# Kernel optimization log

Measured on AMD Instinct MI355X. Metric: run time of the kernel, lower is better.

Reference implementation:

```python
import jax, jax.numpy as jnp
import numpy as np

D = 1024      # embed_size
H = 16        # num_heads
NEXP = 8      # num_experts
TOPK = 3
THRESH = 0.05
COEF = 0.01
B, SQ, SKV = 4, 1024, 1024


def _ln(x, g, b, eps=1e-5):
    m = jnp.mean(x, axis=-1, keepdims=True)
    v = jnp.mean(jnp.square(x - m), axis=-1, keepdims=True)
    return (x - m) * jax.lax.rsqrt(v + eps) * g + b


def setup_inputs() -> dict:
    key = jax.random.key(0)
    ks = jax.random.split(key, 20)
    s = 0.02
    w = lambda k, shape: (jax.random.normal(k, shape, jnp.float32) * s)
    return {
        'query': jax.random.normal(ks[0], (B, SQ, D), jnp.float32),
        'key_value': jax.random.normal(ks[1], (B, SKV, D), jnp.float32),
        'Wq': w(ks[2], (D, D)), 'bq': jnp.zeros((D,), jnp.float32),
        'Wk': w(ks[3], (D, D)), 'bk': jnp.zeros((D,), jnp.float32),
        'Wv': w(ks[4], (D, D)), 'bv': jnp.zeros((D,), jnp.float32),
        'W_in': w(ks[5], (3 * D, D)), 'b_in': jnp.zeros((3 * D,), jnp.float32),
        'W_out': w(ks[6], (D, D)), 'b_out': jnp.zeros((D,), jnp.float32),
        'Wa': w(ks[7], (D, D)), 'ba': jnp.zeros((D,), jnp.float32),
        'ln1_g': jnp.ones((D,), jnp.float32), 'ln1_b': jnp.zeros((D,), jnp.float32),
        'Wg': w(ks[8], (D, NEXP)),
        'ew1': w(ks[9], (NEXP, D, 4 * D)), 'eb1': jnp.zeros((NEXP, 4 * D), jnp.float32),
        'ew2': w(ks[10], (NEXP, 4 * D, D)), 'eb2': jnp.zeros((NEXP, D), jnp.float32),
        'ln2_g': jnp.ones((D,), jnp.float32), 'ln2_b': jnp.zeros((D,), jnp.float32),
    }


def reference(query, key_value, Wq, bq, Wk, bk, Wv, bv, W_in, b_in, W_out, b_out,
              Wa, ba, ln1_g, ln1_b, Wg, ew1, eb1, ew2, eb2, ln2_g, ln2_b):
    Bq, Sq, _ = query.shape
    Skv = key_value.shape[1]
    Dh = D // H
    # outer Q/K/V linears (torch Linear: x @ W.T + b)
    q = query @ Wq.T + bq
    k = key_value @ Wk.T + bk
    v = key_value @ Wv.T + bv
    # nn.MultiheadAttention in-projection
    Wiq, Wik, Wiv = jnp.split(W_in, 3, axis=0)
    biq, bik, biv = jnp.split(b_in, 3)
    qh = (q @ Wiq.T + biq).reshape(Bq, Sq, H, Dh).transpose(0, 2, 1, 3)
    kh = (k @ Wik.T + bik).reshape(Bq, Skv, H, Dh).transpose(0, 2, 1, 3)
    vh = (v @ Wiv.T + biv).reshape(Bq, Skv, H, Dh).transpose(0, 2, 1, 3)
    scores = jnp.einsum('bhqd,bhkd->bhqk', qh, kh) / jnp.sqrt(jnp.float32(Dh))
    attn = jax.nn.softmax(scores, axis=-1)
    o = jnp.einsum('bhqk,bhkd->bhqd', attn, vh).transpose(0, 2, 1, 3).reshape(Bq, Sq, D)
    o = o @ W_out.T + b_out
    # adapt + residual + first_norm
    x = _ln(o @ Wa.T + ba + query, ln1_g, ln1_b)
    # ---- MoE: top-3 softmax gating, threshold on non-top-1 gates ----
    probs = jax.nn.softmax(x @ Wg, axis=-1)                 # [B,S,E]
    topv, topi = jax.lax.top_k(probs, TOPK)                  # [B,S,3]
    keep = jnp.concatenate([jnp.ones_like(topv[..., :1], bool),
                            topv[..., 1:] >= THRESH], axis=-1)
    topv = jnp.where(keep, topv, 0.0)
    combine = jnp.sum(jax.nn.one_hot(topi, NEXP, dtype=x.dtype) * topv[..., None], axis=-2)  # [B,S,E]
    moe_out = jnp.zeros_like(x)
    for e in range(NEXP):  # small fixed expert count
        h = jax.nn.gelu(x @ ew1[e] + eb1[e], approximate=False)
        moe_out = moe_out + combine[..., e:e + 1] * (h @ ew2[e] + eb2[e])
    # load-balance aux loss: E * sum(frac_routed * mean_prob) * coef
    fe = jnp.mean((combine > 0).astype(x.dtype), axis=(0, 1))
    me = jnp.mean(probs, axis=(0, 1))
    aux = COEF * NEXP * jnp.sum(fe * me)
    out = _ln(moe_out + x, ln2_g, ln2_b)
    return out, aux
```

## Files before the change

### kernel.cpp

```cpp
#include <hip/hip_runtime.h>
#include <math.h>

#define THRESH_C 0.05f
#define COEF_C   0.01f

typedef __bf16 bf16;
typedef __bf16 bf16x8 __attribute__((ext_vector_type(8)));
typedef __bf16 bf16x4 __attribute__((ext_vector_type(4)));
typedef float  f32x4  __attribute__((ext_vector_type(4)));

__device__ __forceinline__ void ld16(void* lds_base, const void* g) {
    __builtin_amdgcn_global_load_lds(
        (const __attribute__((address_space(1))) void*)g,
        (__attribute__((address_space(3))) void*)lds_base,
        16, 0, 0);
}

__global__ __launch_bounds__(256) void k_f32_to_split(const float* __restrict__ in,
                                                      bf16* __restrict__ hi,
                                                      bf16* __restrict__ lo, long n) {
    long i = ((long)blockIdx.x * 256 + threadIdx.x) * 4;
    if (i >= n) return;
    float4 v = *(const float4*)(in + i);
    bf16x4 h, l;
    h[0] = (bf16)v.x; l[0] = (bf16)(v.x - (float)h[0]);
    h[1] = (bf16)v.y; l[1] = (bf16)(v.y - (float)h[1]);
    h[2] = (bf16)v.z; l[2] = (bf16)(v.z - (float)h[2]);
    h[3] = (bf16)v.w; l[3] = (bf16)(v.w - (float)h[3]);
    *(bf16x4*)(hi + i) = h;
    *(bf16x4*)(lo + i) = l;
}

__global__ __launch_bounds__(256) void k_transpose4_split(const float* __restrict__ w0,
                                                          const float* __restrict__ w1,
                                                          const float* __restrict__ w2,
                                                          const float* __restrict__ w3,
                                                          bf16* __restrict__ oh,
                                                          bf16* __restrict__ ol) {
    __shared__ float t[64][65];
    int z = blockIdx.z;
    const float* in = (z == 0) ? w0 : (z == 1) ? w1 : (z == 2) ? w2 : w3;
    bf16* ohz = oh + (long)z * 1048576;
    bf16* olz = ol + (long)z * 1048576;
    int r0 = blockIdx.y * 64, c0 = blockIdx.x * 64;
    for (int i = threadIdx.x; i < 4096; i += 256) {
        int r = i >> 6, c = i & 63;
        t[r][c] = in[(long)(r0 + r) * 1024 + (c0 + c)];
    }
    __syncthreads();
    for (int i = threadIdx.x; i < 4096; i += 256) {
        int c = i >> 6, r = i & 63;
        float v = t[r][c];
        bf16 h = (bf16)v;
        long o = (long)(c0 + c) * 1024 + (r0 + r);
        ohz[o] = h;
        olz[o] = (bf16)(v - (float)h);
    }
}

__global__ __launch_bounds__(256) void k_transpose_ew(const float* __restrict__ in,
                                                      bf16* __restrict__ out,
                                                      int R, int C) {
    __shared__ bf16 t[64][65];
    const float* ib = in + (long)blockIdx.z * R * C;
    bf16* ob = out + (long)blockIdx.z * R * C;
    int r0 = blockIdx.y * 64, c0 = blockIdx.x * 64;
    for (int i = threadIdx.x; i < 4096; i += 256) {
        int r = i >> 6, c = i & 63;
        t[r][c] = (bf16)ib[(long)(r0 + r) * C + (c0 + c)];
    }
    __syncthreads();
    for (int i = threadIdx.x; i < 4096; i += 256) {
        int c = i >> 6, r = i & 63;
        ob[(long)(c0 + c) * R + (r0 + r)] = t[r][c];
    }
}

__global__ __launch_bounds__(256) void k_bias_fold4(const float* __restrict__ W_in,
                                                    const float* __restrict__ Wa,
                                                    const float* __restrict__ bq,
                                                    const float* __restrict__ bk,
                                                    const float* __restrict__ bv,
                                                    const float* __restrict__ b_out,
                                                    const float* __restrict__ b_in,
                                                    const float* __restrict__ ba,
                                                    float* __restrict__ y) {
    int z = blockIdx.y;
    const float* W  = (z < 3) ? (W_in + (long)z * 1048576) : Wa;
    const float* b1 = (z == 0) ? bq : (z == 1) ? bk : (z == 2) ? bv : b_out;
    const float* b2 = (z < 3) ? (b_in + z * 1024) : ba;
    int row = blockIdx.x * 4 + (threadIdx.x >> 6);
    int lane = threadIdx.x & 63;
    const float* wr = W + (long)row * 1024;
    float s = 0.f;
    for (int k = lane; k < 1024; k += 64) s += wr[k] * b1[k];
#pragma unroll
    for (int o = 32; o >= 1; o >>= 1) s += __shfl_xor(s, o);
    if (lane == 0) y[z * 1024 + row] = b2[row] + s;
}

enum { HP_SPLIT = 0, HP_F32 = 1, HP_SPLIT_HEADS = 2 };

template<int MODE>
__global__ __launch_bounds__(256)
void gemm_hp(const bf16* __restrict__ Ah, const bf16* __restrict__ Al, int lda, long sAz,
             const bf16* __restrict__ Bh, const bf16* __restrict__ Bl, int ldb, long sBz,
             void* __restrict__ Chv, bf16* __restrict__ Cl, int ldc, long sCz,
             const float* __restrict__ bias, float alpha, int M, int N, int K) {
    __shared__ alignas(16) bf16 sAh[128 * 32];
    __shared__ alignas(16) bf16 sAl[128 * 32];
    __shared__ alignas(16) bf16 sBh[128 * 32];
    __shared__ alignas(16) bf16 sBl[128 * 32];
    const int bm = blockIdx.y, bn = blockIdx.x, z = blockIdx.z;
    const int tid  = threadIdx.x;
    const int lane = tid & 63, wave = tid >> 6;
    const int quad = lane >> 4, l16 = lane & 15;
    const int wr = wave >> 1, wc = wave & 1;
    const int sr = tid >> 2;
    const int sc = (tid & 3) * 8;

    int arow0 = min(bm * 128 + sr, M - 1);
    int arow1 = min(bm * 128 + sr + 64, M - 1);
    int brow0 = min(bn * 128 + sr, N - 1);
    int brow1 = min(bn * 128 + sr + 64, N - 1);

    const bf16* pAh0 = Ah + (long)z * sAz + (long)arow0 * lda + sc;
    const bf16* pAh1 = Ah + (long)z * sAz + (long)arow1 * lda + sc;
    const bf16* pAl0 = Al + (long)z * sAz + (long)arow0 * lda + sc;
    const bf16* pAl1 = Al + (long)z * sAz + (long)arow1 * lda + sc;
    const bf16* pBh0 = Bh + (long)z * sBz + (long)brow0 * ldb + sc;
    const bf16* pBh1 = Bh + (long)z * sBz + (long)brow1 * ldb + sc;
    const bf16* pBl0 = Bl + (long)z * sBz + (long)brow0 * ldb + sc;
    const bf16* pBl1 = Bl + (long)z * sBz + (long)brow1 * ldb + sc;
    const int wo = wave << 9;

    f32x4 acc[4][4];
#pragma unroll
    for (int i = 0; i < 4; i++)
#pragma unroll
        for (int j = 0; j < 4; j++) acc[i][j] = (f32x4){0.f, 0.f, 0.f, 0.f};

    for (int k0 = 0; k0 < K; k0 += 32) {
        __syncthreads();
        ld16(sAh + wo,        pAh0 + k0);
        ld16(sAh + 2048 + wo, pAh1 + k0);
        ld16(sAl + wo,        pAl0 + k0);
        ld16(sAl + 2048 + wo, pAl1 + k0);
        ld16(sBh + wo,        pBh0 + k0);
        ld16(sBh + 2048 + wo, pBh1 + k0);
        ld16(sBl + wo,        pBl0 + k0);
        ld16(sBl + 2048 + wo, pBl1 + k0);
        __syncthreads();
        bf16x8 ah[4], al[4], bh[4], bl[4];
#pragma unroll
        for (int i = 0; i < 4; i++) {
            int ro = (wr * 64 + i * 16 + l16) * 32 + quad * 8;
            ah[i] = *(const bf16x8*)&sAh[ro];
            al[i] = *(const bf16x8*)&sAl[ro];
        }
#pragma unroll
        for (int j = 0; j < 4; j++) {
            int ro = (wc * 64 + j * 16 + l16) * 32 + quad * 8;
            bh[j] = *(const bf16x8*)&sBh[ro];
            bl[j] = *(const bf16x8*)&sBl[ro];
        }
#pragma unroll
        for (int i = 0; i < 4; i++)
#pragma unroll
            for (int j = 0; j < 4; j++) {
                acc[i][j] = __builtin_amdgcn_mfma_f32_16x16x32_bf16(al[i], bh[j], acc[i][j], 0, 0, 0);
                acc[i][j] = __builtin_amdgcn_mfma_f32_16x16x32_bf16(ah[i], bl[j], acc[i][j], 0, 0, 0);
                acc[i][j] = __builtin_amdgcn_mfma_f32_16x16x32_bf16(ah[i], bh[j], acc[i][j], 0, 0, 0);
            }
    }

#pragma unroll
    for (int i = 0; i < 4; i++) {
        int mbase = bm * 128 + wr * 64 + i * 16 + quad * 4;
#pragma unroll
        for (int j = 0; j < 4; j++) {
            int n = bn * 128 + wc * 64 + j * 16 + l16;
            if (n < N) {
                float bv = bias ? bias[n] : 0.f;
#pragma unroll
                for (int r = 0; r < 4; r++) {
                    int m = mbase + r;
                    if (m < M) {
                        float v = alpha * acc[i][j][r] + bv;
                        if (MODE == HP_SPLIT) {
                            long cidx = (long)z * sCz + (long)m * ldc + n;
                            bf16 h = (bf16)v;
                            ((bf16*)Chv)[cidx] = h;
                            Cl[cidx] = (bf16)(v - (float)h);
                        } else if (MODE == HP_F32) {
                            long cidx = (long)z * sCz + (long)m * ldc + n;
                            ((float*)Chv)[cidx] = v;
                        } else {
                            int slice = ((m >> 10) << 4) + (n >> 6);
                            long idx = (long)slice * 65536 + (long)(m & 1023) * 64 + (n & 63);
                            bf16 h = (bf16)v;
                            ((bf16*)Chv)[idx] = h;
                            Cl[idx] = (bf16)(v - (float)h);
                        }
                    }
                }
            }
        }
    }
}

__global__ __launch_bounds__(256)
void gemm_pv(const bf16* __restrict__ Ph, const bf16* __restrict__ Pl,
             const bf16* __restrict__ Vh, const bf16* __restrict__ Vl,
             bf16* __restrict__ Oh, bf16* __restrict__ Ol) {
    __shared__ alignas(16) bf16 sAh[128 * 32];
    __shared__ alignas(16) bf16 sAl[128 * 32];
    __shared__ alignas(16) bf16 sBh[64 * 32];
    __shared__ alignas(16) bf16 sBl[64 * 32];
    const int bm = blockIdx.x, z = blockIdx.y;
    const int tid = threadIdx.x, lane = tid & 63, wave = tid >> 6;
    const int quad = lane >> 4, l16 = lane & 15;
    const int wr = wave & 1, wc = wave >> 1;
    const int sr = tid >> 2, sc = (tid & 3) * 8;

    const bf16* pA0h = Ph + (long)z * 1048576 + (long)(bm * 128 + sr) * 1024 + sc;
    const bf16* pA1h = pA0h + 64 * 1024;
    const bf16* pA0l = Pl + (long)z * 1048576 + (long)(bm * 128 + sr) * 1024 + sc;
    const bf16* pA1l = pA0l + 64 * 1024;
    const bf16* pB0h = Vh + (long)z * 65536 + (long)sr * 1024 + sc;
    const bf16* pB0l = Vl + (long)z * 65536 + (long)sr * 1024 + sc;
    const int wo = wave << 9;
    const int wob = wave << 7;

    f32x4 acc[4][2];
#pragma unroll
    for (int i = 0; i < 4; i++)
#pragma unroll
        for (int j = 0; j < 2; j++) acc[i][j] = (f32x4){0.f, 0.f, 0.f, 0.f};

    for (int k0 = 0; k0 < 1024; k0 += 32) {
        __syncthreads();
        ld16(sAh + wo,        pA0h + k0);
        ld16(sAh + 2048 + wo, pA1h + k0);
        ld16(sAl + wo,        pA0l + k0);
        ld16(sAl + 2048 + wo, pA1l + k0);
        ld16(sBh + wo, pB0h + k0);
        ld16(sBl + wo, pB0l + k0);
        __syncthreads();
        bf16x8 ah[4], al[4], bh[2], bl[2];
#pragma unroll
        for (int i = 0; i < 4; i++) {
            int ro = (wr * 64 + i * 16 + l16) * 32 + quad * 8;
            ah[i] = *(const bf16x8*)&sAh[ro];
            al[i] = *(const bf16x8*)&sAl[ro];
        }
#pragma unroll
        for (int j = 0; j < 2; j++) {
            int ro = (wc * 32 + j * 16 + l16) * 32 + quad * 8;
            bh[j] = *(const bf16x8*)&sBh[ro];
            bl[j] = *(const bf16x8*)&sBl[ro];
        }
#pragma unroll
        for (int i = 0; i < 4; i++)
#pragma unroll
            for (int j = 0; j < 2; j++) {
                acc[i][j] = __builtin_amdgcn_mfma_f32_16x16x32_bf16(al[i], bh[j], acc[i][j], 0, 0, 0);
                acc[i][j] = __builtin_amdgcn_mfma_f32_16x16x32_bf16(ah[i], bl[j], acc[i][j], 0, 0, 0);
                acc[i][j] = __builtin_amdgcn_mfma_f32_16x16x32_bf16(ah[i], bh[j], acc[i][j], 0, 0, 0);
            }
    }

#pragma unroll
    for (int i = 0; i < 4; i++) {
        int mbase = bm * 128 + wr * 64 + i * 16 + quad * 4;
#pragma unroll
        for (int j = 0; j < 2; j++) {
            int n = wc * 32 + j * 16 + l16;
#pragma unroll
            for (int r = 0; r < 4; r++) {
                int m = mbase + r;
                long idx = (long)z * 65536 + (long)m * 64 + n;
                float v = acc[i][j][r];
                bf16 h = (bf16)v;
                Oh[idx] = h;
                Ol[idx] = (bf16)(v - (float)h);
            }
        }
    }
}

__global__ __launch_bounds__(256)
void gemm_moe1(const bf16* __restrict__ Ae, const bf16* __restrict__ ew1t,
               const float* __restrict__ eb1, bf16* __restrict__ Hp,
               const int* __restrict__ counts, const int* __restrict__ bases) {
    const int e = blockIdx.z;
    const int M = counts[e];
    const int bm = blockIdx.y, bn = blockIdx.x;
    if (bm * 128 >= M) return;
    const bf16* A = Ae + (long)bases[e] * 1024;
    const bf16* B = ew1t + (long)e * 4194304;
    bf16* C = Hp + (long)bases[e] * 4096;
    const float* bias = eb1 + e * 4096;

    __shared__ alignas(16) bf16 sA[128 * 32];
    __shared__ alignas(16) bf16 sB[128 * 32];
    const int tid  = threadIdx.x;
    const int lane = tid & 63, wave = tid >> 6;
    const int quad = lane >> 4, l16 = lane & 15;
    const int wr = wave >> 1, wc = wave & 1;
    const int sr = tid >> 2;
    const int sc = (tid & 3) * 8;

    int arow0 = min(bm * 128 + sr, M - 1);
    int arow1 = min(bm * 128 + sr + 64, M - 1);
    int brow0 = bn * 128 + sr;
    const bf16* pA0 = A + (long)arow0 * 1024 + sc;
    const bf16* pA1 = A + (long)arow1 * 1024 + sc;
    const bf16* pB0 = B + (long)brow0 * 1024 + sc;
    const bf16* pB1 = B + (long)(brow0 + 64) * 1024 + sc;
    const int wo = wave << 9;

    f32x4 acc[4][4];
#pragma unroll
    for (int i = 0; i < 4; i++)
#pragma unroll
        for (int j = 0; j < 4; j++) acc[i][j] = (f32x4){0.f, 0.f, 0.f, 0.f};

    for (int k0 = 0; k0 < 1024; k0 += 32) {
        __syncthreads();
        ld16(sA + wo,        pA0 + k0);
        ld16(sA + 2048 + wo, pA1 + k0);
        ld16(sB + wo,        pB0 + k0);
        ld16(sB + 2048 + wo, pB1 + k0);
        __syncthreads();
        bf16x8 af[4], bfr[4];
#pragma unroll
        for (int i = 0; i < 4; i++)
            af[i] = *(const bf16x8*)&sA[(wr * 64 + i * 16 + l16) * 32 + quad * 8];
#pragma unroll
        for (int j = 0; j < 4; j++)
            bfr[j] = *(const bf16x8*)&sB[(wc * 64 + j * 16 + l16) * 32 + quad * 8];
#pragma unroll
        for (int i = 0; i < 4; i++)
#pragma unroll
            for (int j = 0; j < 4; j++)
                acc[i][j] = __builtin_amdgcn_mfma_f32_16x16x32_bf16(af[i], bfr[j], acc[i][j], 0, 0, 0);
    }

#pragma unroll
    for (int i = 0; i < 4; i++) {
        int mbase = bm * 128 + wr * 64 + i * 16 + quad * 4;
#pragma unroll
        for (int j = 0; j < 4; j++) {
            int n = bn * 128 + wc * 64 + j * 16 + l16;
            float bv = bias[n];
#pragma unroll
            for (int r = 0; r < 4; r++) {
                int m = mbase + r;
                if (m < M) {
                    float v = acc[i][j][r] + bv;
                    float g = 0.5f * v * (1.f + erff(v * 0.70710678118654752f));
                    C[(long)m * 4096 + n] = (bf16)g;
                }
            }
        }
    }
}

__global__ __launch_bounds__(256)
void gemm_moe2(const bf16* __restrict__ Hp, const bf16* __restrict__ ew2t,
               const float* __restrict__ eb2, float* __restrict__ moe_out,
               const int* __restrict__ counts, const int* __restrict__ bases,
               const int* __restrict__ tok, const float* __restrict__ combine) {
    const int e = blockIdx.z;
    const int M = counts[e];
    const int ks = blockIdx.y & 3;
    const int bm = blockIdx.y >> 2;
    const int bn = blockIdx.x;
    if (bm * 128 >= M) return;
    const bf16* A = Hp + (long)bases[e] * 4096 + ks * 1024;
    const bf16* B = ew2t + (long)e * 4194304 + ks * 1024;
    const float* bias = eb2 + e * 1024;
    const int* etok = tok + e * 4096;

    __shared__ alignas(16) bf16 sA[128 * 32];
    __shared__ alignas(16) bf16 sB[128 * 32];
    const int tid  = threadIdx.x;
    const int lane = tid & 63, wave = tid >> 6;
    const int quad = lane >> 4, l16 = lane & 15;
    const int wr = wave >> 1, wc = wave & 1;
    const int sr = tid >> 2;
    const int sc = (tid & 3) * 8;

    int arow0 = min(bm * 128 + sr, M - 1);
    int arow1 = min(bm * 128 + sr + 64, M - 1);
    int brow0 = bn * 128 + sr;
    const bf16* pA0 = A + (long)arow0 * 4096 + sc;
    const bf16* pA1 = A + (long)arow1 * 4096 + sc;
    const bf16* pB0 = B + (long)brow0 * 4096 + sc;
    const bf16* pB1 = B + (long)(brow0 + 64) * 4096 + sc;
    const int wo = wave << 9;

    f32x4 acc[4][4];
#pragma unroll
    for (int i = 0; i < 4; i++)
#pragma unroll
        for (int j = 0; j < 4; j++) acc[i][j] = (f32x4){0.f, 0.f, 0.f, 0.f};

    for (int k0 = 0; k0 < 1024; k0 += 32) {
        __syncthreads();
        ld16(sA + wo,        pA0 + k0);
        ld16(sA + 2048 + wo, pA1 + k0);
        ld16(sB + wo,        pB0 + k0);
        ld16(sB + 2048 + wo, pB1 + k0);
        __syncthreads();
        bf16x8 af[4], bfr[4];
#pragma unroll
        for (int i = 0; i < 4; i++)
            af[i] = *(const bf16x8*)&sA[(wr * 64 + i * 16 + l16) * 32 + quad * 8];
#pragma unroll
        for (int j = 0; j < 4; j++)
            bfr[j] = *(const bf16x8*)&sB[(wc * 64 + j * 16 + l16) * 32 + quad * 8];
#pragma unroll
        for (int i = 0; i < 4; i++)
#pragma unroll
            for (int j = 0; j < 4; j++)
                acc[i][j] = __builtin_amdgcn_mfma_f32_16x16x32_bf16(af[i], bfr[j], acc[i][j], 0, 0, 0);
    }

#pragma unroll
    for (int i = 0; i < 4; i++) {
        int mbase = bm * 128 + wr * 64 + i * 16 + quad * 4;
#pragma unroll
        for (int j = 0; j < 4; j++) {
            int n = bn * 128 + wc * 64 + j * 16 + l16;
            float bv = (ks == 0) ? bias[n] : 0.f;
#pragma unroll
            for (int r = 0; r < 4; r++) {
                int m = mbase + r;
                if (m < M) {
                    int t = etok[m];
                    float s = combine[t * 8 + e];
                    atomicAdd(&moe_out[(long)t * 1024 + n], s * (acc[i][j][r] + bv));
                }
            }
        }
    }
}

__global__ __launch_bounds__(256) void k_vsplit(const bf16* __restrict__ VH_h,
                                                const bf16* __restrict__ VH_l,
                                                bf16* __restrict__ VT_h,
                                                bf16* __restrict__ VT_l) {
    __shared__ bf16 th[64][65];
    __shared__ bf16 tl[64][65];
    int s = blockIdx.y, q0 = blockIdx.x * 64;
    int b = s >> 4, h = s & 15;
    long ibase = ((long)(b * 1024 + q0)) * 1024 + h * 64;
    for (int i = threadIdx.x; i < 4096; i += 256) {
        int q = i >> 6, d = i & 63;
        th[q][d] = VH_h[ibase + (long)q * 1024 + d];
        tl[q][d] = VH_l[ibase + (long)q * 1024 + d];
    }
    __syncthreads();
    long obase = (long)s * 65536 + q0;
    for (int i = threadIdx.x; i < 4096; i += 256) {
        int d = i >> 6, q = i & 63;
        VT_h[obase + (long)d * 1024 + q] = th[q][d];
        VT_l[obase + (long)d * 1024 + q] = tl[q][d];
    }
}

__global__ __launch_bounds__(256) void k_ocopy(const bf16* __restrict__ Op_h,
                                               const bf16* __restrict__ Op_l,
                                               bf16* __restrict__ O_h,
                                               bf16* __restrict__ O_l) {
    int t = blockIdx.x * 4 + (threadIdx.x >> 6);
    int lane = threadIdx.x & 63;
    int b = t >> 10, q = t & 1023;
    int h = lane >> 2, dd = (lane & 3) * 16;
    long src = ((long)(b * 16 + h)) * 65536 + (long)q * 64 + dd;
    long dst = (long)t * 1024 + h * 64 + dd;
    *(bf16x8*)(O_h + dst)     = *(const bf16x8*)(Op_h + src);
    *(bf16x8*)(O_h + dst + 8) = *(const bf16x8*)(Op_h + src + 8);
    *(bf16x8*)(O_l + dst)     = *(const bf16x8*)(Op_l + src);
    *(bf16x8*)(O_l + dst + 8) = *(const bf16x8*)(Op_l + src + 8);
}

__global__ __launch_bounds__(256) void k_gather(const bf16* __restrict__ Xb,
                                                const int* __restrict__ tok,
                                                const int* __restrict__ counts,
                                                const int* __restrict__ bases,
                                                bf16* __restrict__ Ae) {
    int e = blockIdx.y;
    int cnt = counts[e];
    long base = bases[e];
    for (int i = blockIdx.x; i < cnt; i += gridDim.x) {
        int t = tok[e * 4096 + i];
        const bf16x4* src = (const bf16x4*)(Xb + (long)t * 1024);
        bf16x4* dst = (bf16x4*)(Ae + (base + i) * 1024);
        dst[threadIdx.x] = src[threadIdx.x];
    }
}

__global__ __launch_bounds__(256) void k_softmax_ip(bf16* __restrict__ Sh,
                                                    bf16* __restrict__ Sl) {
    int row = blockIdx.x * 4 + (threadIdx.x >> 6);
    int lane = threadIdx.x & 63;
    long o = (long)row * 1024 + lane * 16;
    bf16x8 h0 = *(const bf16x8*)(Sh + o), h1 = *(const bf16x8*)(Sh + o + 8);
    bf16x8 l0 = *(const bf16x8*)(Sl + o), l1 = *(const bf16x8*)(Sl + o + 8);
    float v[16];
#pragma unroll
    for (int i = 0; i < 8; i++) {
        v[i] = (float)h0[i] + (float)l0[i];
        v[8 + i] = (float)h1[i] + (float)l1[i];
    }
    float mx = v[0];
#pragma unroll
    for (int i = 1; i < 16; i++) mx = fmaxf(mx, v[i]);
#pragma unroll
    for (int of = 32; of >= 1; of >>= 1) mx = fmaxf(mx, __shfl_xor(mx, of));
    float s = 0.f;
#pragma unroll
    for (int i = 0; i < 16; i++) { v[i] = expf(v[i] - mx); s += v[i]; }
#pragma unroll
    for (int of = 32; of >= 1; of >>= 1) s += __shfl_xor(s, of);
    float inv = 1.f / s;
#pragma unroll
    for (int i = 0; i < 8; i++) {
        float a = v[i] * inv;
        h0[i] = (bf16)a; l0[i] = (bf16)(a - (float)h0[i]);
        float b = v[8 + i] * inv;
        h1[i] = (bf16)b; l1[i] = (bf16)(b - (float)h1[i]);
    }
    *(bf16x8*)(Sh + o) = h0;  *(bf16x8*)(Sh + o + 8) = h1;
    *(bf16x8*)(Sl + o) = l0;  *(bf16x8*)(Sl + o + 8) = l1;
}

__global__ __launch_bounds__(256) void k_ln(const float* __restrict__ xin,
                                            const float* __restrict__ resid,
                                            const float* __restrict__ g,
                                            const float* __restrict__ bb,
                                            float* __restrict__ outf,
                                            bf16* __restrict__ outb) {
    int row = blockIdx.x * 4 + (threadIdx.x >> 6);
    int lane = threadIdx.x & 63;
    long base = (long)row * 1024 + lane * 16;
    float v[16];
#pragma unroll
    for (int i = 0; i < 16; i += 4) {
        f32x4 a = *(const f32x4*)(xin + base + i);
        if (resid) { f32x4 r4 = *(const f32x4*)(resid + base + i); a += r4; }
        v[i] = a[0]; v[i + 1] = a[1]; v[i + 2] = a[2]; v[i + 3] = a[3];
    }
    float s = 0.f;
#pragma unroll
    for (int i = 0; i < 16; i++) s += v[i];
#pragma unroll
    for (int o = 32; o >= 1; o >>= 1) s += __shfl_xor(s, o);
    float mean = s * (1.f / 1024.f);
    float vs = 0.f;
#pragma unroll
    for (int i = 0; i < 16; i++) { float d = v[i] - mean; vs += d * d; }
#pragma unroll
    for (int o = 32; o >= 1; o >>= 1) vs += __shfl_xor(vs, o);
    float inv = 1.f / sqrtf(vs * (1.f / 1024.f) + 1e-5f);
    const float* gp = g + lane * 16;
    const float* bp = bb + lane * 16;
#pragma unroll
    for (int i = 0; i < 16; i++) {
        float o = (v[i] - mean) * inv * gp[i] + bp[i];
        if (outf) outf[base + i] = o;
        if (outb) outb[base + i] = (bf16)o;
    }
}

__global__ __launch_bounds__(256) void k_gate(const float* __restrict__ X,
                                              const float* __restrict__ Wg,
                                              float* __restrict__ combine,
                                              float* __restrict__ partials) {
    __shared__ float sm[16];
    if (threadIdx.x < 16) sm[threadIdx.x] = 0.f;
    __syncthreads();
    int t = blockIdx.x * 4 + (threadIdx.x >> 6);
    int lane = threadIdx.x & 63;
    const float* x = X + (long)t * 1024;
    float acc[8] = {0.f, 0.f, 0.f, 0.f, 0.f, 0.f, 0.f, 0.f};
    for (int i = lane; i < 1024; i += 64) {
        float xv = x[i];
        const float* w = Wg + i * 8;
#pragma unroll
        for (int e = 0; e < 8; e++) acc[e] += xv * w[e];
    }
#pragma unroll
    for (int e = 0; e < 8; e++)
#pragma unroll
        for (int o = 32; o >= 1; o >>= 1) acc[e] += __shfl_xor(acc[e], o);
    if (lane == 0) {
        float mx = acc[0];
#pragma unroll
        for (int e = 1; e < 8; e++) mx = fmaxf(mx, acc[e]);
        float p[8], s = 0.f;
#pragma unroll
        for (int e = 0; e < 8; e++) { p[e] = expf(acc[e] - mx); s += p[e]; }
        float invs = 1.f / s;
#pragma unroll
        for (int e = 0; e < 8; e++) p[e] *= invs;
        float b1 = -1.f, b2 = -1.f, b3 = -1.f; int i1 = 0, i2 = 0, i3 = 0;
#pragma unroll
        for (int e = 0; e < 8; e++) {
            float pe = p[e];
            if (pe > b1)      { b3 = b2; i3 = i2; b2 = b1; i2 = i1; b1 = pe; i1 = e; }
            else if (pe > b2) { b3 = b2; i3 = i2; b2 = pe; i2 = e; }
            else if (pe > b3) { b3 = pe; i3 = e; }
        }
        float c[8] = {0.f, 0.f, 0.f, 0.f, 0.f, 0.f, 0.f, 0.f};
        c[i1] = b1;
        if (b2 >= THRESH_C) c[i2] = b2;
        if (b3 >= THRESH_C) c[i3] = b3;
        float* co = combine + (long)t * 8;
#pragma unroll
        for (int e = 0; e < 8; e++) co[e] = c[e];
#pragma unroll
        for (int e = 0; e < 8; e++) {
            atomicAdd(&sm[e], p[e]);
            if (c[e] > 0.f) atomicAdd(&sm[8 + e], 1.f);
        }
    }
    __syncthreads();
    if (threadIdx.x < 16) partials[(long)blockIdx.x * 16 + threadIdx.x] = sm[threadIdx.x];
}

__global__ __launch_bounds__(256) void k_route(const float* __restrict__ combine,
                                               int* __restrict__ counts,
                                               int* __restrict__ bases,
                                               int* __restrict__ tok) {
    __shared__ int scan[256];
    __shared__ int ebase;
    int tid = threadIdx.x;
    if (tid == 0) ebase = 0;
    __syncthreads();
    for (int e = 0; e < 8; e++) {
        int pred[16]; int cnt = 0;
#pragma unroll
        for (int j = 0; j < 16; j++) {
            int t = tid * 16 + j;
            pred[j] = combine[t * 8 + e] > 0.f ? 1 : 0;
            cnt += pred[j];
        }
        scan[tid] = cnt;
        __syncthreads();
        for (int off = 1; off < 256; off <<= 1) {
            int v = (tid >= off) ? scan[tid - off] : 0;
            __syncthreads();
            scan[tid] += v;
            __syncthreads();
        }
        int o = e * 4096 + scan[tid] - cnt;
        int total = scan[255];
#pragma unroll
        for (int j = 0; j < 16; j++) {
            if (pred[j]) tok[o++] = tid * 16 + j;
        }
        if (tid == 0) { counts[e] = total; bases[e] = ebase; ebase += total; }
        __syncthreads();
    }
}

__global__ __launch_bounds__(256) void k_aux(const float* __restrict__ partials, int nblocks,
                                             float* __restrict__ auxout) {
    __shared__ float red[256];
    int tid = threadIdx.x;
    int e = tid & 15, grp = tid >> 4;
    float s = 0.f;
    for (int b = grp; b < nblocks; b += 16) s += partials[(long)b * 16 + e];
    red[tid] = s;
    __syncthreads();
    if (grp == 0) {
        float tot = 0.f;
        for (int g2 = 0; g2 < 16; g2++) tot += red[g2 * 16 + e];
        red[tid] = tot;
    }
    __syncthreads();
    if (tid == 0) {
        float s2 = 0.f;
        for (int e2 = 0; e2 < 8; e2++)
            s2 += (red[8 + e2] * (1.f / 4096.f)) * (red[e2] * (1.f / 4096.f));
        auxout[0] = COEF_C * 8.f * s2;
    }
}

extern "C" void kernel_launch(void* const* d_in, const int* in_sizes, int n_in,
                              void* d_out, int out_size, void* d_ws, size_t ws_size,
                              hipStream_t stream) {
    const float* query     = (const float*)d_in[0];
    const float* key_value = (const float*)d_in[1];
    const float* Wq   = (const float*)d_in[2];
    const float* bq   = (const float*)d_in[3];
    const float* Wk   = (const float*)d_in[4];
    const float* bk   = (const float*)d_in[5];
    const float* Wv   = (const float*)d_in[6];
    const float* bv   = (const float*)d_in[7];
    const float* W_in = (const float*)d_in[8];
    const float* b_in = (const float*)d_in[9];
    const float* W_out = (const float*)d_in[10];
    const float* b_out = (const float*)d_in[11];
    const float* Wa   = (const float*)d_in[12];
    const float* ba   = (const float*)d_in[13];
    const float* ln1_g = (const float*)d_in[14];
    const float* ln1_b = (const float*)d_in[15];
    const float* Wg   = (const float*)d_in[16];
    const float* ew1  = (const float*)d_in[17];
    const float* eb1  = (const float*)d_in[18];
    const float* ew2  = (const float*)d_in[19];
    const float* eb2  = (const float*)d_in[20];
    const float* ln2_g = (const float*)d_in[21];
    const float* ln2_b = (const float*)d_in[22];

    const size_t MBY = 1ull << 20;
    const long MB1 = 1024L * 1024L;
    char* ws = (char*)d_ws;

    bf16* Sh   = (bf16*)(ws + 0 * MBY);
    bf16* Sl   = (bf16*)(ws + 64 * MBY);
    bf16* ew1t = (bf16*)(ws + 0 * MBY);
    bf16* ew2t = (bf16*)(ws + 64 * MBY);
    bf16* WAll_h = (bf16*)(ws + 128 * MBY);
    bf16* WAll_l = (bf16*)(ws + 136 * MBY);
    bf16* WT_h   = (bf16*)(ws + 144 * MBY);
    bf16* WT_l   = (bf16*)(ws + 152 * MBY);
    bf16* Xq_h  = (bf16*)(ws + 160 * MBY), *Xq_l  = (bf16*)(ws + 168 * MBY);
    bf16* Xkv_h = (bf16*)(ws + 176 * MBY), *Xkv_l = (bf16*)(ws + 184 * MBY);
    bf16* O_h  = (bf16*)(ws + 160 * MBY), *O_l  = (bf16*)(ws + 168 * MBY);
    bf16* QHp_h = (bf16*)(ws + 192 * MBY), *QHp_l = (bf16*)(ws + 200 * MBY);
    bf16* KHp_h = (bf16*)(ws + 208 * MBY), *KHp_l = (bf16*)(ws + 216 * MBY);
    bf16* VH_h  = (bf16*)(ws + 224 * MBY), *VH_l  = (bf16*)(ws + 232 * MBY);
    bf16* VTp_h = (bf16*)(ws + 240 * MBY), *VTp_l = (bf16*)(ws + 248 * MBY);
    bf16* Op_h  = (bf16*)(ws + 256 * MBY), *Op_l  = (bf16*)(ws + 264 * MBY);
    float* Xf   = (float*)(ws + 256 * MBY);
    float* Af   = (float*)(ws + 272 * MBY);
    bf16* Ae      = (bf16*)(ws + 128 * MBY);
    bf16* Hp      = (bf16*)(ws + 152 * MBY);
    float* moe_out = (float*)(ws + 272 * MBY);
    bf16* Xb   = (bf16*)(ws + 320 * MBY);
    bf16* Weff_h = (bf16*)(ws + 328 * MBY);
    bf16* Weff_l = (bf16*)(ws + 336 * MBY);
    float* combine  = (float*)(ws + 344 * MBY);
    float* partials = (float*)(ws + 344 * MBY + 128 * 1024);
    float* beff     = (float*)(ws + 344 * MBY + 192 * 1024);
    int*   counts   = (int*)  (ws + 344 * MBY + 212 * 1024);
    int*   bases    = (int*)  (ws + 344 * MBY + 213 * 1024);
    int*   tok      = (int*)  (ws + 344 * MBY + 214 * 1024);

    dim3 blk(256);

    k_f32_to_split<<<4096, blk, 0, stream>>>(query, Xq_h, Xq_l, 4L * MB1);
    k_f32_to_split<<<4096, blk, 0, stream>>>(key_value, Xkv_h, Xkv_l, 4L * MB1);
    k_f32_to_split<<<3072, blk, 0, stream>>>(W_in, WAll_h, WAll_l, 3L * MB1);
    k_f32_to_split<<<1024, blk, 0, stream>>>(Wa, WAll_h + 3 * MB1, WAll_l + 3 * MB1, MB1);
    k_transpose4_split<<<dim3(16, 16, 4), blk, 0, stream>>>(Wq, Wk, Wv, W_out, WT_h, WT_l);
    k_bias_fold4<<<dim3(256, 4), blk, 0, stream>>>(W_in, Wa, bq, bk, bv, b_out, b_in, ba, beff);

    gemm_hp<HP_SPLIT><<<dim3(8, 8, 4), blk, 0, stream>>>(
        WAll_h, WAll_l, 1024, MB1, WT_h, WT_l, 1024, MB1,
        Weff_h, Weff_l, 1024, MB1, nullptr, 1.f, 1024, 1024, 1024);

    dim3 gP(8, 32, 1);
    gemm_hp<HP_SPLIT_HEADS><<<gP, blk, 0, stream>>>(Xq_h, Xq_l, 1024, 0, Weff_h, Weff_l, 1024, 0,
                                                    QHp_h, QHp_l, 0, 0, beff, 1.f, 4096, 1024, 1024);
    gemm_hp<HP_SPLIT_HEADS><<<gP, blk, 0, stream>>>(Xkv_h, Xkv_l, 1024, 0, Weff_h + MB1, Weff_l + MB1, 1024, 0,
                                                    KHp_h, KHp_l, 0, 0, beff + 1024, 1.f, 4096, 1024, 1024);
    gemm_hp<HP_SPLIT><<<gP, blk, 0, stream>>>(Xkv_h, Xkv_l, 1024, 0, Weff_h + 2 * MB1, Weff_l + 2 * MB1, 1024, 0,
                                              VH_h, VH_l, 1024, 0, beff + 2048, 1.f, 4096, 1024, 1024);
    k_vsplit<<<dim3(16, 64), blk, 0, stream>>>(VH_h, VH_l, VTp_h, VTp_l);

    for (int half = 0; half < 2; half++) {
        long so = (long)half * 32 * 65536;
        gemm_hp<HP_SPLIT><<<dim3(8, 8, 32), blk, 0, stream>>>(
            QHp_h + so, QHp_l + so, 64, 65536,
            KHp_h + so, KHp_l + so, 64, 65536,
            Sh, Sl, 1024, MB1, nullptr, 0.125f, 1024, 1024, 64);
        k_softmax_ip<<<8192, blk, 0, stream>>>(Sh, Sl);
        gemm_pv<<<dim3(8, 32), blk, 0, stream>>>(Sh, Sl, VTp_h + so, VTp_l + so,
                                                 Op_h + so, Op_l + so);
    }
    k_ocopy<<<1024, blk, 0, stream>>>(Op_h, Op_l, O_h, O_l);

    gemm_hp<HP_F32><<<gP, blk, 0, stream>>>(O_h, O_l, 1024, 0, Weff_h + 3 * MB1, Weff_l + 3 * MB1, 1024, 0,
                                            Af, nullptr, 1024, 0, beff + 3072, 1.f, 4096, 1024, 1024);
    k_ln<<<1024, blk, 0, stream>>>(Af, query, ln1_g, ln1_b, Xf, Xb);
    k_gate<<<1024, blk, 0, stream>>>(Xf, Wg, combine, partials);
    k_route<<<1, blk, 0, stream>>>(combine, counts, bases, tok);
    k_gather<<<dim3(512, 8), blk, 0, stream>>>(Xb, tok, counts, bases, Ae);

    k_transpose_ew<<<dim3(64, 16, 8), blk, 0, stream>>>(ew1, ew1t, 1024, 4096);
    k_transpose_ew<<<dim3(16, 64, 8), blk, 0, stream>>>(ew2, ew2t, 4096, 1024);

    hipMemsetAsync(moe_out, 0, (long)4096 * 1024 * 4, stream);
    gemm_moe1<<<dim3(32, 32, 8), blk, 0, stream>>>(Ae, ew1t, eb1, Hp, counts, bases);
    gemm_moe2<<<dim3(8, 128, 8), blk, 0, stream>>>(Hp, ew2t, eb2, moe_out, counts, bases, tok, combine);

    k_ln<<<1024, blk, 0, stream>>>(moe_out, Xf, ln2_g, ln2_b, (float*)d_out, nullptr);
    k_aux<<<1, blk, 0, stream>>>(partials, 1024, (float*)d_out + (out_size - 1));
}
```

Before: 1.751 ms.

## Replace atomic scatter in MoE down-projection with dense store and fused combine+LayerNorm

The second expert GEMM no longer splits K four ways and scatters weighted results into moe_out with float atomics. It now runs the full K=4096 reduction per tile and writes plain per-expert rows into a compacted buffer. The router also emits a token-to-slot map, which a new kernel uses to gather each token's expert outputs, add bias, apply the gate weights and the residual, and run LayerNorm. This removes the memset and the atomic traffic, but the GEMM grid is four times smaller and each block runs a longer K loop, so there is less parallelism.

```diff
diff --git a/kernel.cpp b/kernel.cpp
--- a/kernel.cpp
+++ b/kernel.cpp
@@ -230,7 +230,6 @@
     const bf16* pB0h = Vh + (long)z * 65536 + (long)sr * 1024 + sc;
     const bf16* pB0l = Vl + (long)z * 65536 + (long)sr * 1024 + sc;
     const int wo = wave << 9;
-    const int wob = wave << 7;
 
     f32x4 acc[4][2];
 #pragma unroll
@@ -369,19 +368,16 @@
 
 __global__ __launch_bounds__(256)
 void gemm_moe2(const bf16* __restrict__ Hp, const bf16* __restrict__ ew2t,
-               const float* __restrict__ eb2, float* __restrict__ moe_out,
-               const int* __restrict__ counts, const int* __restrict__ bases,
-               const int* __restrict__ tok, const float* __restrict__ combine) {
+               float* __restrict__ Y,
+               const int* __restrict__ counts, const int* __restrict__ bases) {
     const int e = blockIdx.z;
     const int M = counts[e];
-    const int ks = blockIdx.y & 3;
-    const int bm = blockIdx.y >> 2;
+    const int bm = blockIdx.y;
     const int bn = blockIdx.x;
     if (bm * 128 >= M) return;
-    const bf16* A = Hp + (long)bases[e] * 4096 + ks * 1024;
-    const bf16* B = ew2t + (long)e * 4194304 + ks * 1024;
-    const float* bias = eb2 + e * 1024;
-    const int* etok = tok + e * 4096;
+    const bf16* A = Hp + (long)bases[e] * 4096;
+    const bf16* B = ew2t + (long)e * 4194304;
+    float* C = Y + (long)bases[e] * 1024;
 
     __shared__ alignas(16) bf16 sA[128 * 32];
     __shared__ alignas(16) bf16 sB[128 * 32];
@@ -407,7 +403,7 @@
 #pragma unroll
         for (int j = 0; j < 4; j++) acc[i][j] = (f32x4){0.f, 0.f, 0.f, 0.f};
 
-    for (int k0 = 0; k0 < 1024; k0 += 32) {
+    for (int k0 = 0; k0 < 4096; k0 += 32) {
         __syncthreads();
         ld16(sA + wo,        pA0 + k0);
         ld16(sA + 2048 + wo, pA1 + k0);
@@ -434,15 +430,10 @@
 #pragma unroll
         for (int j = 0; j < 4; j++) {
             int n = bn * 128 + wc * 64 + j * 16 + l16;
-            float bv = (ks == 0) ? bias[n] : 0.f;
 #pragma unroll
             for (int r = 0; r < 4; r++) {
                 int m = mbase + r;
-                if (m < M) {
-                    int t = etok[m];
-                    float s = combine[t * 8 + e];
-                    atomicAdd(&moe_out[(long)t * 1024 + n], s * (acc[i][j][r] + bv));
-                }
+                if (m < M) C[(long)m * 1024 + n] = acc[i][j][r];
             }
         }
     }
@@ -576,6 +567,59 @@
     }
 }
 
+__global__ __launch_bounds__(256) void k_moe_ln(const float* __restrict__ Y,
+                                                const int* __restrict__ pos,
+                                                const float* __restrict__ combine,
+                                                const float* __restrict__ eb2,
+                                                const float* __restrict__ resid,
+                                                const float* __restrict__ g,
+                                                const float* __restrict__ bb,
+                                                float* __restrict__ outf) {
+    int row = blockIdx.x * 4 + (threadIdx.x >> 6);
+    int lane = threadIdx.x & 63;
+    long base = (long)row * 1024 + lane * 16;
+    float v[16];
+#pragma unroll
+    for (int i = 0; i < 16; i += 4) {
+        f32x4 a = *(const f32x4*)(resid + base + i);
+        v[i] = a[0]; v[i + 1] = a[1]; v[i + 2] = a[2]; v[i + 3] = a[3];
+    }
+    for (int e = 0; e < 8; e++) {
+        int p = pos[row * 8 + e];
+        if (p >= 0) {
+            float c = combine[row * 8 + e];
+            const float* yr = Y + (long)p * 1024 + lane * 16;
+            const float* br = eb2 + e * 1024 + lane * 16;
+#pragma unroll
+            for (int i = 0; i < 16; i += 4) {
+                f32x4 y4 = *(const f32x4*)(yr + i);
+                f32x4 b4 = *(const f32x4*)(br + i);
+                v[i]     += c * (y4[0] + b4[0]);
+                v[i + 1] += c * (y4[1] + b4[1]);
+                v[i + 2] += c * (y4[2] + b4[2]);
+                v[i + 3] += c * (y4[3] + b4[3]);
+            }
+        }
+    }
+    float s = 0.f;
+#pragma unroll
+    for (int i = 0; i < 16; i++) s += v[i];
+#pragma unroll
+    for (int o = 32; o >= 1; o >>= 1) s += __shfl_xor(s, o);
+    float mean = s * (1.f / 1024.f);
+    float vs = 0.f;
+#pragma unroll
+    for (int i = 0; i < 16; i++) { float d = v[i] - mean; vs += d * d; }
+#pragma unroll
+    for (int o = 32; o >= 1; o >>= 1) vs += __shfl_xor(vs, o);
+    float inv = 1.f / sqrtf(vs * (1.f / 1024.f) + 1e-5f);
+    const float* gp = g + lane * 16;
+    const float* bp = bb + lane * 16;
+#pragma unroll
+    for (int i = 0; i < 16; i++)
+        outf[base + i] = (v[i] - mean) * inv * gp[i] + bp[i];
+}
+
 __global__ __launch_bounds__(256) void k_gate(const float* __restrict__ X,
                                               const float* __restrict__ Wg,
                                               float* __restrict__ combine,
@@ -635,12 +679,11 @@
 __global__ __launch_bounds__(256) void k_route(const float* __restrict__ combine,
                                                int* __restrict__ counts,
                                                int* __restrict__ bases,
-                                               int* __restrict__ tok) {
+                                               int* __restrict__ tok,
+                                               int* __restrict__ pos) {
     __shared__ int scan[256];
-    __shared__ int ebase;
     int tid = threadIdx.x;
-    if (tid == 0) ebase = 0;
-    __syncthreads();
+    int mybase = 0;
     for (int e = 0; e < 8; e++) {
         int pred[16]; int cnt = 0;
 #pragma unroll
@@ -657,13 +700,18 @@
             scan[tid] += v;
             __syncthreads();
         }
-        int o = e * 4096 + scan[tid] - cnt;
+        int start = scan[tid] - cnt;
         int total = scan[255];
+        int o = e * 4096 + start;
+        int gp = mybase + start;
 #pragma unroll
         for (int j = 0; j < 16; j++) {
-            if (pred[j]) tok[o++] = tid * 16 + j;
-        }
-        if (tid == 0) { counts[e] = total; bases[e] = ebase; ebase += total; }
+            int t = tid * 16 + j;
+            if (pred[j]) { tok[o++] = t; pos[t * 8 + e] = gp++; }
+            else pos[t * 8 + e] = -1;
+        }
+        if (tid == 0) { counts[e] = total; bases[e] = mybase; }
+        mybase += total;
         __syncthreads();
     }
 }
@@ -742,7 +790,7 @@
     float* Af   = (float*)(ws + 272 * MBY);
     bf16* Ae      = (bf16*)(ws + 128 * MBY);
     bf16* Hp      = (bf16*)(ws + 152 * MBY);
-    float* moe_out = (float*)(ws + 272 * MBY);
+    float* Yp     = (float*)(ws + 272 * MBY);
     bf16* Xb   = (bf16*)(ws + 320 * MBY);
     bf16* Weff_h = (bf16*)(ws + 328 * MBY);
     bf16* Weff_l = (bf16*)(ws + 336 * MBY);
@@ -752,6 +800,7 @@
     int*   counts   = (int*)  (ws + 344 * MBY + 212 * 1024);
     int*   bases    = (int*)  (ws + 344 * MBY + 213 * 1024);
     int*   tok      = (int*)  (ws + 344 * MBY + 214 * 1024);
+    int*   pos      = (int*)  (ws + 344 * MBY + 342 * 1024);
 
     dim3 blk(256);
 
@@ -791,16 +840,15 @@
                                             Af, nullptr, 1024, 0, beff + 3072, 1.f, 4096, 1024, 1024);
     k_ln<<<1024, blk, 0, stream>>>(Af, query, ln1_g, ln1_b, Xf, Xb);
     k_gate<<<1024, blk, 0, stream>>>(Xf, Wg, combine, partials);
-    k_route<<<1, blk, 0, stream>>>(combine, counts, bases, tok);
+    k_route<<<1, blk, 0, stream>>>(combine, counts, bases, tok, pos);
     k_gather<<<dim3(512, 8), blk, 0, stream>>>(Xb, tok, counts, bases, Ae);
 
     k_transpose_ew<<<dim3(64, 16, 8), blk, 0, stream>>>(ew1, ew1t, 1024, 4096);
     k_transpose_ew<<<dim3(16, 64, 8), blk, 0, stream>>>(ew2, ew2t, 4096, 1024);
 
-    hipMemsetAsync(moe_out, 0, (long)4096 * 1024 * 4, stream);
     gemm_moe1<<<dim3(32, 32, 8), blk, 0, stream>>>(Ae, ew1t, eb1, Hp, counts, bases);
-    gemm_moe2<<<dim3(8, 128, 8), blk, 0, stream>>>(Hp, ew2t, eb2, moe_out, counts, bases, tok, combine);
-
-    k_ln<<<1024, blk, 0, stream>>>(moe_out, Xf, ln2_g, ln2_b, (float*)d_out, nullptr);
+    gemm_moe2<<<dim3(8, 32, 8), blk, 0, stream>>>(Hp, ew2t, Yp, counts, bases);
+
+    k_moe_ln<<<1024, blk, 0, stream>>>(Yp, pos, combine, eb2, Xf, ln2_g, ln2_b, (float*)d_out);
     k_aux<<<1, blk, 0, stream>>>(partials, 1024, (float*)d_out + (out_size - 1));
 }
```

After: 1.603 ms. 8.4% less time.
